# Kernel optimization log

Hardware: AMD Instinct MI355X
Metric: run time of the kernel (lower is better)

## Reference

```python
import jax, jax.numpy as jnp
import numpy as np

ALPHA = 0.5
B = 4096
K = 8192


def setup_inputs() -> dict:
    key = jax.random.key(0)
    k1, k2 = jax.random.split(key)
    outputs = jax.random.normal(k1, (B, K), dtype=jnp.float32)
    labels = jax.random.randint(k2, (B,), 0, K)
    targets = jax.nn.one_hot(labels, K, dtype=jnp.float32)
    S = jnp.eye(K, dtype=jnp.float32)          # soft-label matrix (state)
    S_t = jnp.zeros((K, K), dtype=jnp.float32)  # running stats (state)
    count = jnp.zeros((K, 1), dtype=jnp.float32)
    return {"outputs": outputs, "targets": targets, "S": S, "S_t": S_t, "count": count}


def reference(outputs, targets, S, S_t, count):
    # loss path
    ls = jax.nn.log_softmax(outputs, axis=1)          # [B, K]
    bsz = outputs.shape[0]
    target_label = jnp.argmax(targets, axis=1)        # [B]
    prediction = jnp.argmax(outputs, axis=1)          # [B]
    soft_targets = S[target_label]                    # [B, K] gather
    ce_hard = -(ls * targets).sum() / bsz
    ce_soft = -(ls * soft_targets).sum() / bsz
    loss = ALPHA * ce_hard + (1.0 - ALPHA) * ce_soft

    # stats accumulation (the original python for-loop, as one fused scatter-add)
    probs = jax.nn.softmax(jax.lax.stop_gradient(outputs), axis=1)  # [B, K]
    correct = (prediction == target_label).astype(probs.dtype)      # [B]
    S_t_new = S_t + jax.ops.segment_sum(probs * correct[:, None], target_label, num_segments=K)
    count_new = count + jax.ops.segment_sum(correct, target_label, num_segments=K)[:, None]
    return loss, S_t_new, count_new
```

## Files before the change

kernel.cpp:

```cpp
#include <hip/hip_runtime.h>
#include <math.h>

#define K 8192
#define BROWS 4096
#define ALPHA 0.5f
#define NTOT ((size_t)K * (size_t)K)
#define VEC4 16777215

typedef float f32x4 __attribute__((ext_vector_type(4)));

__device__ __forceinline__ void argmax_combine(float& v, int& i, float v2, int i2){
  if (v2 > v || (v2 == v && i2 < i)) { v = v2; i = i2; }
}

__global__ __launch_bounds__(256) void fused_kernel(
    const float* __restrict__ outputs,
    const float* __restrict__ targets,
    const float* __restrict__ S,
    const float* __restrict__ S_t,
    const float* __restrict__ count,
    float* __restrict__ out,
    float* __restrict__ rowloss,
    int*   __restrict__ rowtl,
    int*   __restrict__ rowcorrect,
    float* __restrict__ rowm,
    float* __restrict__ rowinvZ)
{
  __shared__ float s_v[2][4]; __shared__ int s_i[2][4];
  __shared__ float s_m; __shared__ int s_pred; __shared__ int s_tl;
  __shared__ float s_sums[4][5];

  const int bb = blockIdx.x;
  const int r  = bb / 3;
  const int m3 = bb - r * 3;
  const int t  = threadIdx.x;
  const int lane = t & 63;
  const int wid  = t >> 6;

  if (m3 != 0) {
    const int cb = 2 * r + (m3 - 1);
    const f32x4* src4 = (const f32x4*)S_t;
    f32x4* dst4 = (f32x4*)(out + 4);
    const size_t base = (size_t)cb * 2048 + t;
    if (cb != 8191) {
#pragma unroll
      for (int i = 0; i < 8; ++i) {
        size_t d = base + (size_t)i * 256;
        f32x4 a = src4[d];
        float nx = __shfl_down(a.x, 1, 64);
        float ny = __shfl_down(a.y, 1, 64);
        float nz = __shfl_down(a.z, 1, 64);
        if (lane == 63) {
          f32x4 e = src4[d + 1];
          nx = e.x; ny = e.y; nz = e.z;
        }
        f32x4 v; v.x = a.w; v.y = nx; v.z = ny; v.w = nz;
        __builtin_nontemporal_store(v, &dst4[d]);
      }
    } else {
#pragma unroll
      for (int i = 0; i < 8; ++i) {
        size_t d = base + (size_t)i * 256;
        f32x4 a = src4[d];
        float nx = __shfl_down(a.x, 1, 64);
        float ny = __shfl_down(a.y, 1, 64);
        float nz = __shfl_down(a.z, 1, 64);
        bool instore = d < (size_t)VEC4;
        if (lane == 63 && instore) {
          f32x4 e = src4[d + 1];
          nx = e.x; ny = e.y; nz = e.z;
        }
        if (instore) {
          f32x4 v; v.x = a.w; v.y = nx; v.z = ny; v.w = nz;
          __builtin_nontemporal_store(v, &dst4[d]);
        }
      }
    }
    if (cb == 0) {
      if (t < 3) out[1 + t] = S_t[t];
      if (t == 3) out[NTOT] = S_t[NTOT - 1];
    } else if (cb == 1) {
      float* out_count = out + 1 + NTOT;
      for (int i = t; i < K; i += 256) out_count[i] = count[i];
    }
    return;
  }

  const float4* orow = (const float4*)(outputs + (size_t)r * K);
  float x[32];
#pragma unroll
  for (int i = 0; i < 8; ++i){
    float4 v = orow[i*256 + t];
    x[4*i+0]=v.x; x[4*i+1]=v.y; x[4*i+2]=v.z; x[4*i+3]=v.w;
  }

  float mv = -INFINITY; int mi = 0x7fffffff;
#pragma unroll
  for (int i = 0; i < 8; ++i){
#pragma unroll
    for (int c = 0; c < 4; ++c){
      int idx = i*1024 + t*4 + c;
      argmax_combine(mv, mi, x[4*i+c], idx);
    }
  }

  const float4* trow = (const float4*)(targets + (size_t)r * K);
  float tv = -INFINITY; int ti = 0x7fffffff;
  float d_hard = 0.f, s_hard = 0.f;
#pragma unroll
  for (int i = 0; i < 8; ++i){
    float4 v = trow[i*256 + t];
    float tc[4] = {v.x, v.y, v.z, v.w};
#pragma unroll
    for (int c = 0; c < 4; ++c){
      int idx = i*1024 + t*4 + c;
      d_hard += x[4*i+c] * tc[c];
      s_hard += tc[c];
      argmax_combine(tv, ti, tc[c], idx);
    }
  }

#pragma unroll
  for (int off = 32; off; off >>= 1){
    float v2 = __shfl_down(mv, off, 64); int i2 = __shfl_down(mi, off, 64);
    argmax_combine(mv, mi, v2, i2);
    v2 = __shfl_down(tv, off, 64); i2 = __shfl_down(ti, off, 64);
    argmax_combine(tv, ti, v2, i2);
  }

  if (lane == 0){ s_v[0][wid]=mv; s_i[0][wid]=mi; s_v[1][wid]=tv; s_i[1][wid]=ti; }
  __syncthreads();
  if (t == 0){
    float av=s_v[0][0]; int ai=s_i[0][0];
    float bv=s_v[1][0]; int bi=s_i[1][0];
#pragma unroll
    for (int w=1; w<4; ++w){
      argmax_combine(av, ai, s_v[0][w], s_i[0][w]);
      argmax_combine(bv, bi, s_v[1][w], s_i[1][w]);
    }
    s_m = av; s_pred = ai; s_tl = bi;
  }
  __syncthreads();
  const float m  = s_m;
  const int   tl = s_tl;

  float se = 0.f;
#pragma unroll
  for (int i = 0; i < 32; ++i) se += expf(x[i] - m);

  const float4* srow = (const float4*)(S + (size_t)tl * K);
  float d_soft = 0.f, s_soft = 0.f;
#pragma unroll
  for (int i = 0; i < 8; ++i){
    float4 v = srow[i*256 + t];
    d_soft += x[4*i+0]*v.x + x[4*i+1]*v.y + x[4*i+2]*v.z + x[4*i+3]*v.w;
    s_soft += v.x + v.y + v.z + v.w;
  }

  float sums[5] = {d_hard, s_hard, se, d_soft, s_soft};
#pragma unroll
  for (int off = 32; off; off >>= 1){
#pragma unroll
    for (int j = 0; j < 5; ++j) sums[j] += __shfl_down(sums[j], off, 64);
  }
  if (lane == 0){
#pragma unroll
    for (int j = 0; j < 5; ++j) s_sums[wid][j] = sums[j];
  }
  __syncthreads();
  if (t == 0){
    float tot[5];
#pragma unroll
    for (int j=0;j<5;++j) tot[j] = s_sums[0][j]+s_sums[1][j]+s_sums[2][j]+s_sums[3][j];
    float Z = tot[2];
    float logZ = logf(Z);
    float ceh = -(tot[0] - (m + logZ) * tot[1]);
    float ces = -(tot[3] - (m + logZ) * tot[4]);
    rowloss[r]    = (ALPHA * ceh + (1.0f - ALPHA) * ces) * (1.0f / (float)BROWS);
    rowtl[r]      = tl;
    rowcorrect[r] = (s_pred == tl) ? 1 : 0;
    rowm[r]       = m;
    rowinvZ[r]    = 1.0f / Z;
  }
}

__global__ __launch_bounds__(256) void epilogue_kernel(
    const float* __restrict__ outputs,
    const float* __restrict__ rowloss,
    const int*   __restrict__ rowtl,
    const int*   __restrict__ rowcorrect,
    const float* __restrict__ rowm,
    const float* __restrict__ rowinvZ,
    float* __restrict__ out)
{
  const int b = blockIdx.x;
  const int t = threadIdx.x;
  if (b == BROWS) {
    float s = 0.f;
    for (int i = t; i < BROWS; i += 256) s += rowloss[i];
#pragma unroll
    for (int off = 32; off; off >>= 1) s += __shfl_down(s, off, 64);
    __shared__ float sh[4];
    if ((t & 63) == 0) sh[t >> 6] = s;
    __syncthreads();
    if (t == 0) out[0] = sh[0] + sh[1] + sh[2] + sh[3];
    return;
  }
  if (!rowcorrect[b]) return;
  const int tl = rowtl[b];
  const float m = rowm[b], invZ = rowinvZ[b];
  const float* orow = outputs + (size_t)b * K;
  float* drow = out + 1 + (size_t)tl * K;
  for (int k = t; k < K; k += 256)
    atomicAdd(&drow[k], expf(orow[k] - m) * invZ);
  if (t == 0) atomicAdd(out + 1 + NTOT + tl, 1.0f);
}

extern "C" void kernel_launch(void* const* d_in, const int* in_sizes, int n_in,
                              void* d_out, int out_size, void* d_ws, size_t ws_size,
                              hipStream_t stream) {
  const float* outputs = (const float*)d_in[0];
  const float* targets = (const float*)d_in[1];
  const float* S       = (const float*)d_in[2];
  const float* S_t     = (const float*)d_in[3];
  const float* count   = (const float*)d_in[4];

  float* out = (float*)d_out;

  float* rowloss    = (float*)d_ws;
  float* rowm       = rowloss + BROWS;
  float* rowinvZ    = rowm + BROWS;
  int*   rowtl      = (int*)(rowinvZ + BROWS);
  int*   rowcorrect = rowtl + BROWS;

  hipLaunchKernelGGL(fused_kernel, dim3(3 * BROWS), dim3(256), 0, stream,
                     outputs, targets, S, S_t, count, out,
                     rowloss, rowtl, rowcorrect, rowm, rowinvZ);
  hipLaunchKernelGGL(epilogue_kernel, dim3(BROWS + 1), dim3(256), 0, stream,
                     outputs, rowloss, rowtl, rowcorrect, rowm, rowinvZ, out);
}
```

Before: 724.6 us.

## Use persistent grid with grid-strided S_t copy and two rows per block

Replaces the 3*BROWS-block launch, where blocks were split between copying S_t and per-row loss work, with 2048 blocks. Each block first copies a grid-strided slice of S_t, issuing eight loads before the stores to raise memory-level parallelism, then handles two loss rows. The intent is to cut block scheduling overhead, give every block the same mix of work, and keep more loads in flight. In exchange each thread does more serial work, and the per-element bounds check now runs on every iteration.

After: 766.6 us. 1.06x slower.

```diff
diff --git a/kernel.cpp b/kernel.cpp
--- a/kernel.cpp
+++ b/kernel.cpp
@@ -6,6 +6,8 @@
 #define ALPHA 0.5f
 #define NTOT ((size_t)K * (size_t)K)
 #define VEC4 16777215
+#define NBLK 2048
+#define TOTTH ((size_t)NBLK * 256)
 
 typedef float f32x4 __attribute__((ext_vector_type(4)));
 
@@ -31,156 +33,145 @@
   __shared__ float s_sums[4][5];
 
   const int bb = blockIdx.x;
-  const int r  = bb / 3;
-  const int m3 = bb - r * 3;
   const int t  = threadIdx.x;
   const int lane = t & 63;
   const int wid  = t >> 6;
-
-  if (m3 != 0) {
-    const int cb = 2 * r + (m3 - 1);
+  const size_t tid = (size_t)bb * 256 + t;
+
+  {
     const f32x4* src4 = (const f32x4*)S_t;
     f32x4* dst4 = (f32x4*)(out + 4);
-    const size_t base = (size_t)cb * 2048 + t;
-    if (cb != 8191) {
+#pragma unroll
+    for (int outer = 0; outer < 4; ++outer) {
+      const size_t d0 = tid + (size_t)outer * 8 * TOTTH;
+      f32x4 a[8];
+#pragma unroll
+      for (int i = 0; i < 8; ++i) a[i] = src4[d0 + (size_t)i * TOTTH];
 #pragma unroll
       for (int i = 0; i < 8; ++i) {
-        size_t d = base + (size_t)i * 256;
-        f32x4 a = src4[d];
-        float nx = __shfl_down(a.x, 1, 64);
-        float ny = __shfl_down(a.y, 1, 64);
-        float nz = __shfl_down(a.z, 1, 64);
-        if (lane == 63) {
-          f32x4 e = src4[d + 1];
-          nx = e.x; ny = e.y; nz = e.z;
-        }
-        f32x4 v; v.x = a.w; v.y = nx; v.z = ny; v.w = nz;
-        __builtin_nontemporal_store(v, &dst4[d]);
-      }
-    } else {
-#pragma unroll
-      for (int i = 0; i < 8; ++i) {
-        size_t d = base + (size_t)i * 256;
-        f32x4 a = src4[d];
-        float nx = __shfl_down(a.x, 1, 64);
-        float ny = __shfl_down(a.y, 1, 64);
-        float nz = __shfl_down(a.z, 1, 64);
-        bool instore = d < (size_t)VEC4;
+        const size_t d = d0 + (size_t)i * TOTTH;
+        float nx = __shfl_down(a[i].x, 1, 64);
+        float ny = __shfl_down(a[i].y, 1, 64);
+        float nz = __shfl_down(a[i].z, 1, 64);
+        const bool instore = d < (size_t)VEC4;
         if (lane == 63 && instore) {
           f32x4 e = src4[d + 1];
           nx = e.x; ny = e.y; nz = e.z;
         }
         if (instore) {
-          f32x4 v; v.x = a.w; v.y = nx; v.z = ny; v.w = nz;
+          f32x4 v; v.x = a[i].w; v.y = nx; v.z = ny; v.w = nz;
           __builtin_nontemporal_store(v, &dst4[d]);
         }
       }
     }
-    if (cb == 0) {
+    if (bb == 0) {
       if (t < 3) out[1 + t] = S_t[t];
       if (t == 3) out[NTOT] = S_t[NTOT - 1];
-    } else if (cb == 1) {
+    } else if (bb == 1) {
       float* out_count = out + 1 + NTOT;
       for (int i = t; i < K; i += 256) out_count[i] = count[i];
     }
-    return;
   }
 
-  const float4* orow = (const float4*)(outputs + (size_t)r * K);
-  float x[32];
-#pragma unroll
-  for (int i = 0; i < 8; ++i){
-    float4 v = orow[i*256 + t];
-    x[4*i+0]=v.x; x[4*i+1]=v.y; x[4*i+2]=v.z; x[4*i+3]=v.w;
-  }
-
-  float mv = -INFINITY; int mi = 0x7fffffff;
-#pragma unroll
-  for (int i = 0; i < 8; ++i){
-#pragma unroll
-    for (int c = 0; c < 4; ++c){
-      int idx = i*1024 + t*4 + c;
-      argmax_combine(mv, mi, x[4*i+c], idx);
-    }
-  }
-
-  const float4* trow = (const float4*)(targets + (size_t)r * K);
-  float tv = -INFINITY; int ti = 0x7fffffff;
-  float d_hard = 0.f, s_hard = 0.f;
-#pragma unroll
-  for (int i = 0; i < 8; ++i){
-    float4 v = trow[i*256 + t];
-    float tc[4] = {v.x, v.y, v.z, v.w};
-#pragma unroll
-    for (int c = 0; c < 4; ++c){
-      int idx = i*1024 + t*4 + c;
-      d_hard += x[4*i+c] * tc[c];
-      s_hard += tc[c];
-      argmax_combine(tv, ti, tc[c], idx);
-    }
-  }
-
-#pragma unroll
-  for (int off = 32; off; off >>= 1){
-    float v2 = __shfl_down(mv, off, 64); int i2 = __shfl_down(mi, off, 64);
-    argmax_combine(mv, mi, v2, i2);
-    v2 = __shfl_down(tv, off, 64); i2 = __shfl_down(ti, off, 64);
-    argmax_combine(tv, ti, v2, i2);
-  }
-
-  if (lane == 0){ s_v[0][wid]=mv; s_i[0][wid]=mi; s_v[1][wid]=tv; s_i[1][wid]=ti; }
-  __syncthreads();
-  if (t == 0){
-    float av=s_v[0][0]; int ai=s_i[0][0];
-    float bv=s_v[1][0]; int bi=s_i[1][0];
-#pragma unroll
-    for (int w=1; w<4; ++w){
-      argmax_combine(av, ai, s_v[0][w], s_i[0][w]);
-      argmax_combine(bv, bi, s_v[1][w], s_i[1][w]);
-    }
-    s_m = av; s_pred = ai; s_tl = bi;
-  }
-  __syncthreads();
-  const float m  = s_m;
-  const int   tl = s_tl;
-
-  float se = 0.f;
-#pragma unroll
-  for (int i = 0; i < 32; ++i) se += expf(x[i] - m);
-
-  const float4* srow = (const float4*)(S + (size_t)tl * K);
-  float d_soft = 0.f, s_soft = 0.f;
-#pragma unroll
-  for (int i = 0; i < 8; ++i){
-    float4 v = srow[i*256 + t];
-    d_soft += x[4*i+0]*v.x + x[4*i+1]*v.y + x[4*i+2]*v.z + x[4*i+3]*v.w;
-    s_soft += v.x + v.y + v.z + v.w;
-  }
-
-  float sums[5] = {d_hard, s_hard, se, d_soft, s_soft};
-#pragma unroll
-  for (int off = 32; off; off >>= 1){
-#pragma unroll
-    for (int j = 0; j < 5; ++j) sums[j] += __shfl_down(sums[j], off, 64);
-  }
-  if (lane == 0){
-#pragma unroll
-    for (int j = 0; j < 5; ++j) s_sums[wid][j] = sums[j];
-  }
-  __syncthreads();
-  if (t == 0){
-    float tot[5];
-#pragma unroll
-    for (int j=0;j<5;++j) tot[j] = s_sums[0][j]+s_sums[1][j]+s_sums[2][j]+s_sums[3][j];
-    float Z = tot[2];
-    float logZ = logf(Z);
-    float ceh = -(tot[0] - (m + logZ) * tot[1]);
-    float ces = -(tot[3] - (m + logZ) * tot[4]);
-    rowloss[r]    = (ALPHA * ceh + (1.0f - ALPHA) * ces) * (1.0f / (float)BROWS);
-    rowtl[r]      = tl;
-    rowcorrect[r] = (s_pred == tl) ? 1 : 0;
-    rowm[r]       = m;
-    rowinvZ[r]    = 1.0f / Z;
+  for (int rr = 0; rr < 2; ++rr) {
+    const int r = bb + rr * NBLK;
+
+    const float4* orow = (const float4*)(outputs + (size_t)r * K);
+    float x[32];
+#pragma unroll
+    for (int i = 0; i < 8; ++i){
+      float4 v = orow[i*256 + t];
+      x[4*i+0]=v.x; x[4*i+1]=v.y; x[4*i+2]=v.z; x[4*i+3]=v.w;
+    }
+
+    float mv = -INFINITY; int mi = 0x7fffffff;
+#pragma unroll
+    for (int i = 0; i < 8; ++i){
+#pragma unroll
+      for (int c = 0; c < 4; ++c){
+        int idx = i*1024 + t*4 + c;
+        argmax_combine(mv, mi, x[4*i+c], idx);
+      }
+    }
+
+    const float4* trow = (const float4*)(targets + (size_t)r * K);
+    float tv = -INFINITY; int ti = 0x7fffffff;
+    float d_hard = 0.f, s_hard = 0.f;
+#pragma unroll
+    for (int i = 0; i < 8; ++i){
+      float4 v = trow[i*256 + t];
+      float tc[4] = {v.x, v.y, v.z, v.w};
+#pragma unroll
+      for (int c = 0; c < 4; ++c){
+        int idx = i*1024 + t*4 + c;
+        d_hard += x[4*i+c] * tc[c];
+        s_hard += tc[c];
+        argmax_combine(tv, ti, tc[c], idx);
+      }
+    }
+
+#pragma unroll
+    for (int off = 32; off; off >>= 1){
+      float v2 = __shfl_down(mv, off, 64); int i2 = __shfl_down(mi, off, 64);
+      argmax_combine(mv, mi, v2, i2);
+      v2 = __shfl_down(tv, off, 64); i2 = __shfl_down(ti, off, 64);
+      argmax_combine(tv, ti, v2, i2);
+    }
+
+    if (lane == 0){ s_v[0][wid]=mv; s_i[0][wid]=mi; s_v[1][wid]=tv; s_i[1][wid]=ti; }
+    __syncthreads();
+    if (t == 0){
+      float av=s_v[0][0]; int ai=s_i[0][0];
+      float bv=s_v[1][0]; int bi=s_i[1][0];
+#pragma unroll
+      for (int w=1; w<4; ++w){
+        argmax_combine(av, ai, s_v[0][w], s_i[0][w]);
+        argmax_combine(bv, bi, s_v[1][w], s_i[1][w]);
+      }
+      s_m = av; s_pred = ai; s_tl = bi;
+    }
+    __syncthreads();
+    const float m  = s_m;
+    const int   tl = s_tl;
+
+    float se = 0.f;
+#pragma unroll
+    for (int i = 0; i < 32; ++i) se += expf(x[i] - m);
+
+    const float4* srow = (const float4*)(S + (size_t)tl * K);
+    float d_soft = 0.f, s_soft = 0.f;
+#pragma unroll
+    for (int i = 0; i < 8; ++i){
+      float4 v = srow[i*256 + t];
+      d_soft += x[4*i+0]*v.x + x[4*i+1]*v.y + x[4*i+2]*v.z + x[4*i+3]*v.w;
+      s_soft += v.x + v.y + v.z + v.w;
+    }
+
+    float sums[5] = {d_hard, s_hard, se, d_soft, s_soft};
+#pragma unroll
+    for (int off = 32; off; off >>= 1){
+#pragma unroll
+      for (int j = 0; j < 5; ++j) sums[j] += __shfl_down(sums[j], off, 64);
+    }
+    if (lane == 0){
+#pragma unroll
+      for (int j = 0; j < 5; ++j) s_sums[wid][j] = sums[j];
+    }
+    __syncthreads();
+    if (t == 0){
+      float tot[5];
+#pragma unroll
+      for (int j=0;j<5;++j) tot[j] = s_sums[0][j]+s_sums[1][j]+s_sums[2][j]+s_sums[3][j];
+      float Z = tot[2];
+      float logZ = logf(Z);
+      float ceh = -(tot[0] - (m + logZ) * tot[1]);
+      float ces = -(tot[3] - (m + logZ) * tot[4]);
+      rowloss[r]    = (ALPHA * ceh + (1.0f - ALPHA) * ces) * (1.0f / (float)BROWS);
+      rowtl[r]      = tl;
+      rowcorrect[r] = (s_pred == tl) ? 1 : 0;
+      rowm[r]       = m;
+      rowinvZ[r]    = 1.0f / Z;
+    }
   }
 }
 
@@ -233,7 +224,7 @@
   int*   rowtl      = (int*)(rowinvZ + BROWS);
   int*   rowcorrect = rowtl + BROWS;
 
-  hipLaunchKernelGGL(fused_kernel, dim3(3 * BROWS), dim3(256), 0, stream,
+  hipLaunchKernelGGL(fused_kernel, dim3(NBLK), dim3(256), 0, stream,
                      outputs, targets, S, S_t, count, out,
                      rowloss, rowtl, rowcorrect, rowm, rowinvZ);
   hipLaunchKernelGGL(epilogue_kernel, dim3(BROWS + 1), dim3(256), 0, stream,
```
